# Kernel tuning notes

Hardware: AMD Instinct MI355X
Metric: run time of the kernel (lower is better)

Reference implementation:

```python
import jax, jax.numpy as jnp
import numpy as np


def setup_inputs() -> dict:
    key = jax.random.key(0)
    ks = jax.random.split(key, 8)
    B, C, H, W = 16, 256, 64, 64
    E, heads, R = 256, 8, 64
    s = 0.02  # small init scale in lieu of xavier
    return {
        "x": jax.random.normal(ks[0], (B, C, H, W), dtype=jnp.float32),
        "Wqkv": jax.random.normal(ks[1], (3 * E, C), dtype=jnp.float32) * s,
        "bqkv": jnp.zeros((3 * E,), dtype=jnp.float32),
        "Wr": jax.random.normal(ks[2], (2 * R * heads, C), dtype=jnp.float32) * s,
        "br": jnp.zeros((2 * R * heads,), dtype=jnp.float32),
        "Wout": jax.random.normal(ks[3], (C, E), dtype=jnp.float32) * s,
        "bout": jnp.zeros((C,), dtype=jnp.float32),
        "alpha": jax.random.normal(ks[4], (1,), dtype=jnp.float32),
        "num_heads": heads,
        "num_regions": R,
    }


def reference(x, Wqkv, bqkv, Wr, br, Wout, bout, alpha, num_heads, num_regions):
    B, C, H, W = x.shape
    N = H * W
    E = Wqkv.shape[0] // 3
    d = E // num_heads  # head_dim
    xf = x.reshape(B, C, N)  # [B, C, N]

    # qkv 1x1 conv -> [B, 3E, N] -> [B, h, N, 3d] -> q,k,v [B, h, N, d]
    qkv = jnp.einsum("oc,bcn->bon", Wqkv, xf) + bqkv[:, None]
    qkv = qkv.reshape(B, num_heads, 3 * d, N).transpose(0, 1, 3, 2)
    q, k, v = jnp.split(qkv, 3, axis=-1)

    # region projections: 1x1 conv + softmax over the FULL channel axis (2*R*heads)
    r = jnp.einsum("oc,bcn->bon", Wr, xf) + br[:, None]
    r = jax.nn.softmax(r, axis=1)
    r = r.reshape(B, num_heads, 2 * num_regions, N).transpose(0, 1, 3, 2)
    Rq, Rk = jnp.split(r, 2, axis=-1)  # each [B, h, N, R]

    # pool tokens into regions: [B, h, d, R]
    qr = jnp.einsum("bhnd,bhnr->bhdr", q, Rq)
    kr = jnp.einsum("bhnd,bhnr->bhdr", k, Rk)
    vr = jnp.einsum("bhnd,bhnr->bhdr", v, Rk)

    # region-level attention [B, h, Rq, Rk], scaled by sqrt(head_dim)
    logits = jnp.einsum("bhdq,bhdk->bhqk", qr, kr) / jnp.sqrt(jnp.asarray(d, x.dtype))
    attn = jax.nn.softmax(logits, axis=-1)  # dropout is identity at eval

    # values = v_r @ attn^T -> [B, h, d, Rq]; expand back to tokens via Rq^T
    vals = jnp.einsum("bhdk,bhqk->bhdq", vr, attn)
    vals = jnp.einsum("bhdq,bhnq->bhdn", vals, Rq)  # [B, h, d, N]

    vals = vals.reshape(B, E, N)
    out = jnp.einsum("oe,ben->bon", Wout, vals) + bout[:, None]
    out = out.reshape(B, C, H, W)
    return x + alpha * out
```

## Files before the change

### kernel.cpp

```cpp
#include <hip/hip_runtime.h>
#include <cstdint>

typedef unsigned short ushort_t;
typedef __attribute__((ext_vector_type(4))) unsigned short ushort4_t;
typedef __attribute__((ext_vector_type(8))) unsigned short ushort8_t;
typedef __attribute__((ext_vector_type(8))) __bf16 bf16x8;
typedef __attribute__((ext_vector_type(4))) float f32x4;

constexpr int NB = 16;
constexpr int NC = 256;
constexpr int NN = 4096;
constexpr int NP = 1024;
constexpr int NT = 512;
constexpr int NO = 768;

static __device__ __forceinline__ ushort_t f2b(float f) {
  uint32_t u = __builtin_bit_cast(uint32_t, f);
  u += 0x7FFFu + ((u >> 16) & 1u);
  return (ushort_t)(u >> 16);
}
static __device__ __forceinline__ float b2f(ushort_t h) {
  return __builtin_bit_cast(float, (uint32_t)h << 16);
}
static __device__ __forceinline__ f32x4 mfma16(bf16x8 a, bf16x8 b, f32x4 c) {
  return __builtin_amdgcn_mfma_f32_16x16x32_bf16(a, b, c, 0, 0, 0);
}
typedef __attribute__((address_space(1))) const unsigned int guint;
typedef __attribute__((address_space(3))) unsigned int luint;
static __device__ __forceinline__ void glds16(const void* g, void* l) {
  __builtin_amdgcn_global_load_lds((guint*)g, (luint*)l, 16, 0, 0);
}

template <int KITERS>
__device__ __forceinline__ void gemm_core_sb(const ushort_t* __restrict__ Asrc, size_t lda,
                                             const ushort_t* __restrict__ Bsrc, size_t ldb,
                                             ushort_t* SH, f32x4 (&acc)[4][4], int tid) {
  const int l = tid & 63, w = tid >> 6;
  const int fr = l & 15, kq = (l >> 4) * 8;
  const int rr = l >> 3;
  const int sc = ((l & 7) ^ rr) << 3;
  const int swz = (fr & 7) << 3;
  const int wm = (w >> 1) * 64, wn = (w & 1) * 64;
  ushort_t* As = SH;
  ushort_t* Bs = SH + 8192;
#pragma unroll 1
  for (int it = 0; it < KITERS; it++) {
    const size_t k0 = (size_t)it * 64;
#pragma unroll
    for (int i = 0; i < 4; i++) {
      const int row = i * 32 + w * 8 + rr;
      glds16(Asrc + (size_t)row * lda + k0 + sc, As + (i * 32 + w * 8) * 64);
      glds16(Bsrc + (size_t)row * ldb + k0 + sc, Bs + (i * 32 + w * 8) * 64);
    }
    __syncthreads();
#pragma unroll
    for (int ks = 0; ks < 2; ks++) {
      const int col = ks * 32 + kq;
      bf16x8 af[4], bf[4];
#pragma unroll
      for (int f = 0; f < 4; f++) {
        af[f] = *(const bf16x8*)&As[(wm + f * 16 + fr) * 64 + (col ^ swz)];
        bf[f] = *(const bf16x8*)&Bs[(wn + f * 16 + fr) * 64 + (col ^ swz)];
      }
#pragma unroll
      for (int fm = 0; fm < 4; fm++)
#pragma unroll
        for (int fn = 0; fn < 4; fn++)
          acc[fm][fn] = mfma16(af[fm], bf[fn], acc[fm][fn]);
    }
    __syncthreads();
  }
}

__global__ __launch_bounds__(256) void k0_cvt(const float* __restrict__ x,
                                              ushort_t* __restrict__ xb,
                                              ushort_t* __restrict__ xt) {
  __shared__ ushort_t tr[64][88];
  const int tid = threadIdx.x;
  const int n0 = blockIdx.x * 64, c0 = blockIdx.y * 64, b = blockIdx.z;
  const int cr = (tid >> 4) * 4;
  const int nc4 = (tid & 15) * 4;
#pragma unroll
  for (int i = 0; i < 4; i++) {
    size_t idx = ((size_t)b * NC + c0 + cr + i) * NN + n0 + nc4;
    float4 v = *(const float4*)(x + idx);
    ushort4_t o;
    o[0] = f2b(v.x); o[1] = f2b(v.y); o[2] = f2b(v.z); o[3] = f2b(v.w);
    *(ushort4_t*)(xb + idx) = o;
    tr[nc4 + 0][cr + i] = o[0];
    tr[nc4 + 1][cr + i] = o[1];
    tr[nc4 + 2][cr + i] = o[2];
    tr[nc4 + 3][cr + i] = o[3];
  }
  __syncthreads();
  const int nr = tid >> 2, cc0 = (tid & 3) * 16;
  size_t odx = ((size_t)b * NN + n0 + nr) * NC + c0 + cc0;
  *(ushort8_t*)(xt + odx) = *(const ushort8_t*)&tr[nr][cc0];
  *(ushort8_t*)(xt + odx + 8) = *(const ushort8_t*)&tr[nr][cc0 + 8];
}

__global__ __launch_bounds__(256) void cvt_f2b_k(const float* __restrict__ src,
                                                 ushort_t* __restrict__ dst) {
  int i = (blockIdx.x * 256 + threadIdx.x) * 4;
  float4 v = *(const float4*)(src + i);
  ushort4_t o;
  o[0] = f2b(v.x); o[1] = f2b(v.y); o[2] = f2b(v.z); o[3] = f2b(v.w);
  *(ushort4_t*)(dst + i) = o;
}

__global__ __launch_bounds__(512) void k1_proj(const ushort_t* __restrict__ Wrb,
                                               const ushort_t* __restrict__ xt,
                                               const float* __restrict__ br,
                                               ushort_t* __restrict__ P) {
  __shared__ __align__(16) ushort_t SH[32768];
  const int tid = threadIdx.x;
  const int ord = blockIdx.x;
  const int L = (ord & 7) * 128 + (ord >> 3);
  const int m0 = (L & 3) * 256;
  const int n0 = ((L >> 2) & 15) * 256;
  const int b = L >> 6;
  const int l = tid & 63, w = tid >> 6;
  const int wr = w >> 2, wc = w & 3;
  const int fr = l & 15, kq = (l >> 4) * 8;
  const int swz = (fr & 7) << 3;
  ushort_t* As = SH;
  ushort_t* Bs = SH + 16384;
  const ushort_t* Asrc = Wrb + (size_t)m0 * NC;
  const ushort_t* Bsrc = xt + ((size_t)b * NN + n0) * NC;
  f32x4 acc[8][4] = {};
#pragma unroll 1
  for (int k0 = 0; k0 < NC; k0 += 64) {
#pragma unroll
    for (int rnd = 0; rnd < 4; rnd++) {
      const int rbase = rnd * 64 + w * 8;
      const int row = rbase + (l >> 3);
      const int sc = ((l & 7) ^ (row & 7)) << 3;
      glds16(Asrc + (size_t)row * NC + k0 + sc, As + rbase * 64);
      glds16(Bsrc + (size_t)row * NC + k0 + sc, Bs + rbase * 64);
    }
    __syncthreads();
#pragma unroll
    for (int ks = 0; ks < 2; ks++) {
      const int col = ks * 32 + kq;
      bf16x8 af[8], bf[4];
#pragma unroll
      for (int f = 0; f < 8; f++)
        af[f] = *(const bf16x8*)&As[(wr * 128 + f * 16 + fr) * 64 + (col ^ swz)];
#pragma unroll
      for (int f = 0; f < 4; f++)
        bf[f] = *(const bf16x8*)&Bs[(wc * 64 + f * 16 + fr) * 64 + (col ^ swz)];
#pragma unroll
      for (int fm = 0; fm < 8; fm++)
#pragma unroll
        for (int fn = 0; fn < 4; fn++)
          acc[fm][fn] = mfma16(af[fm], bf[fn], acc[fm][fn]);
    }
    __syncthreads();
  }
  const int colc = l & 15, rb = (l >> 4) * 4;
#pragma unroll
  for (int pp = 0; pp < 4; pp++) {
    if (wr == (pp >> 1)) {
      const int fmb = (pp & 1) * 4;
#pragma unroll
      for (int fm = 0; fm < 4; fm++)
#pragma unroll
        for (int rg = 0; rg < 4; rg++) {
          const int rl = fm * 16 + rb + rg;
          const float bias = br[m0 + pp * 64 + rl];
#pragma unroll
          for (int fn = 0; fn < 4; fn++)
            SH[rl * 264 + wc * 64 + fn * 16 + colc] = f2b(acc[fmb + fm][fn][rg] + bias);
        }
    }
    __syncthreads();
    const int orow = tid >> 3, c8 = (tid & 7) * 32;
    ushort_t* dst = P + ((size_t)b * NP + m0 + pp * 64 + orow) * NN + n0 + c8;
    const ushort_t* s = &SH[orow * 264 + c8];
#pragma unroll
    for (int j = 0; j < 4; j++)
      *(ushort8_t*)(dst + j * 8) = *(const ushort8_t*)(s + j * 8);
    __syncthreads();
  }
}

__global__ __launch_bounds__(512) void k2_softmax(ushort_t* __restrict__ P,
                                                  float* __restrict__ sPpart) {
  __shared__ float red[64][64];
  __shared__ float Mf[64], If[64];
  const int tid = threadIdx.x;
  const int n0 = blockIdx.x * 64, b = blockIdx.y;
  const int cg = tid & 7, pg = tid >> 3;
  ushort_t* base = P + (size_t)b * NP * NN + n0 + cg * 8;

  ushort8_t v[16];
  float m[8];
#pragma unroll
  for (int j = 0; j < 8; j++) m[j] = -3.0e38f;
#pragma unroll
  for (int r = 0; r < 16; r++) {
    v[r] = *(const ushort8_t*)(base + (size_t)(pg * 16 + r) * NN);
#pragma unroll
    for (int j = 0; j < 8; j++) m[j] = fmaxf(m[j], b2f(v[r][j]));
  }
#pragma unroll
  for (int j = 0; j < 8; j++) red[pg][cg * 8 + j] = m[j];
  __syncthreads();
  if (tid < 64) {
    float M = -3.0e38f;
    for (int g = 0; g < 64; g++) M = fmaxf(M, red[g][tid]);
    Mf[tid] = M;
  }
  __syncthreads();
  float mj[8], s[8];
#pragma unroll
  for (int j = 0; j < 8; j++) { mj[j] = Mf[cg * 8 + j]; s[j] = 0.f; }
#pragma unroll
  for (int r = 0; r < 16; r++)
#pragma unroll
    for (int j = 0; j < 8; j++) s[j] += __expf(b2f(v[r][j]) - mj[j]);
#pragma unroll
  for (int j = 0; j < 8; j++) red[pg][cg * 8 + j] = s[j];
  __syncthreads();
  if (tid < 64) {
    float S = 0.f;
    for (int g = 0; g < 64; g++) S += red[g][tid];
    If[tid] = 1.f / S;
  }
  __syncthreads();
  float ij[8];
#pragma unroll
  for (int j = 0; j < 8; j++) ij[j] = If[cg * 8 + j];
#pragma unroll
  for (int r = 0; r < 16; r++) {
    int p = pg * 16 + r;
    ushort8_t o;
    float rs = 0.f;
#pragma unroll
    for (int j = 0; j < 8; j++) {
      float e = __expf(b2f(v[r][j]) - mj[j]) * ij[j];
      o[j] = f2b(e);
      rs += e;
    }
    *(ushort8_t*)(base + (size_t)p * NN) = o;
    rs += __shfl_xor(rs, 1, 64);
    rs += __shfl_xor(rs, 2, 64);
    rs += __shfl_xor(rs, 4, 64);
    if (cg == 0) sPpart[((size_t)blockIdx.x * NB + b) * NP + p] = rs;
  }
}

__global__ __launch_bounds__(256) void k2r_reduce(const float* __restrict__ sPpart,
                                                  float* __restrict__ sP) {
  int idx = blockIdx.x * 256 + threadIdx.x;
  float s = 0.f;
#pragma unroll 8
  for (int bx = 0; bx < 64; bx++) s += sPpart[(size_t)bx * (NB * NP) + idx];
  sP[idx] = s;
}

__global__ __launch_bounds__(256) void k3_pool(const ushort_t* __restrict__ xb,
                                               const ushort_t* __restrict__ P,
                                               ushort_t* __restrict__ XRbT) {
  __shared__ __align__(16) ushort_t SH[4 * 8192];
  const int tid = threadIdx.x;
  const int ord = blockIdx.x;
  const int L = (ord & 7) * 32 + (ord >> 3);
  const int m0 = (L & 1) * 128;
  const int n0 = ((L >> 1) & 7) * 128;
  const int b = L >> 4;
  const int l = tid & 63, w = tid >> 6;
  const int fr = l & 15, kq = (l >> 4) * 8;
  const int rr = l >> 3;
  const int sc = ((l & 7) ^ rr) << 3;
  const int swz = (fr & 7) << 3;
  const int wm = (w >> 1) * 64, wn = (w & 1) * 64;
  const ushort_t* Asrc = xb + ((size_t)b * NC + m0) * NN;
  const ushort_t* Bsrc = P + ((size_t)b * NP + n0) * NN;
  f32x4 acc[4][4] = {};

  auto STAGE = [&](int bi, size_t k0) {
    ushort_t* Ad = SH + bi * 8192;
    ushort_t* Bd = SH + 16384 + bi * 8192;
#pragma unroll
    for (int i = 0; i < 4; i++) {
      const int row = i * 32 + w * 8 + rr;
      glds16(Asrc + (size_t)row * NN + k0 + sc, Ad + (i * 32 + w * 8) * 64);
      glds16(Bsrc + (size_t)row * NN + k0 + sc, Bd + (i * 32 + w * 8) * 64);
    }
  };

  STAGE(0, 0);
  __syncthreads();
  int cur = 0;
#pragma unroll 1
  for (int it = 0; it < 64; it++) {
    if (it + 1 < 64) STAGE(cur ^ 1, (size_t)(it + 1) * 64);
    const ushort_t* Ar = SH + cur * 8192;
    const ushort_t* Br = SH + 16384 + cur * 8192;
#pragma unroll
    for (int ks = 0; ks < 2; ks++) {
      const int col = ks * 32 + kq;
      bf16x8 af[4], bf[4];
#pragma unroll
      for (int f = 0; f < 4; f++) {
        af[f] = *(const bf16x8*)&Ar[(wm + f * 16 + fr) * 64 + (col ^ swz)];
        bf[f] = *(const bf16x8*)&Br[(wn + f * 16 + fr) * 64 + (col ^ swz)];
      }
#pragma unroll
      for (int fm = 0; fm < 4; fm++)
#pragma unroll
        for (int fn = 0; fn < 4; fn++)
          acc[fm][fn] = mfma16(af[fm], bf[fn], acc[fm][fn]);
    }
    __syncthreads();
    cur ^= 1;
  }
  const int colc = l & 15, rb = (l >> 4) * 4;
#pragma unroll
  for (int pp = 0; pp < 2; pp++) {
    if ((w & 1) == pp) {
#pragma unroll
      for (int fm = 0; fm < 4; fm++)
#pragma unroll
        for (int rg = 0; rg < 4; rg++) {
          const int cl = wm + fm * 16 + rb + rg;
#pragma unroll
          for (int fn = 0; fn < 4; fn++) {
            const int pl = fn * 16 + colc;
            SH[pl * 136 + cl] = f2b(acc[fm][fn][rg]);
          }
        }
    }
    __syncthreads();
    const int prow = tid >> 2, cch = (tid & 3) * 32;
    ushort_t* dst = XRbT + ((size_t)b * NP + n0 + pp * 64 + prow) * NC + m0 + cch;
    const ushort_t* s = &SH[prow * 136 + cch];
#pragma unroll
    for (int j = 0; j < 4; j++)
      *(ushort8_t*)(dst + j * 8) = *(const ushort8_t*)(s + j * 8);
    __syncthreads();
  }
}

__global__ __launch_bounds__(256) void k4a_qkvr(const ushort_t* __restrict__ Wqkvb,
                                                const ushort_t* __restrict__ XRbT,
                                                const float* __restrict__ bqkv,
                                                const float* __restrict__ sP,
                                                ushort_t* __restrict__ QKVRb) {
  __shared__ __align__(16) ushort_t SH[2 * 8192];
  const int tid = threadIdx.x;
  const int ord = blockIdx.x;
  const int L = (ord & 7) * 96 + (ord >> 3);
  const int m0 = (L % 6) * 128;
  const int rest = L / 6;
  const int n0 = (rest & 7) * 128;
  const int b = rest >> 3;
  const int lane = tid & 63, w = tid >> 6;
  const int wm = (w >> 1) * 64, wn = (w & 1) * 64;
  f32x4 acc[4][4] = {};
  gemm_core_sb<4>(Wqkvb + (size_t)m0 * NC, NC,
                  XRbT + ((size_t)b * NP + n0) * NC, NC, SH, acc, tid);
  const int col = lane & 15, rb = (lane >> 4) * 4;
  float spv[4];
#pragma unroll
  for (int fn = 0; fn < 4; fn++) spv[fn] = sP[(size_t)b * NP + n0 + wn + fn * 16 + col];
#pragma unroll
  for (int fm = 0; fm < 4; fm++)
#pragma unroll
    for (int rg = 0; rg < 4; rg++) {
      int row = m0 + wm + fm * 16 + rb + rg;
      float bq = bqkv[row];
#pragma unroll
      for (int fn = 0; fn < 4; fn++) {
        int cc = n0 + wn + fn * 16 + col;
        QKVRb[((size_t)b * NO + row) * NP + cc] = f2b(acc[fm][fn][rg] + bq * spv[fn]);
      }
    }
}

__global__ __launch_bounds__(256) void k4b_attn(const ushort_t* __restrict__ QKVRb,
                                                const float* __restrict__ Wout,
                                                ushort_t* __restrict__ Tmb) {
  const int b = blockIdx.x >> 3, h = blockIdx.x & 7;
  const int tid = threadIdx.x;
  __shared__ float qf[96][64];
  __shared__ float attn_sT[64][65];
  __shared__ float vals_s[32][64];
#pragma unroll
  for (int i = 0; i < 3; i++) {
    int u = i * 256 + tid;
    int rw = u >> 3, jc = (u & 7) * 8;
    int p0 = h * 128 + ((rw < 32) ? 0 : 64);
    ushort8_t v = *(const ushort8_t*)(QKVRb + ((size_t)b * NO + h * 96 + rw) * NP + p0 + jc);
#pragma unroll
    for (int j = 0; j < 8; j++) qf[rw][jc + j] = b2f(v[j]);
  }
  __syncthreads();
  const int lj = tid & 63;
  const int rq = tid >> 6;
  float kcol[32];
#pragma unroll
  for (int dd = 0; dd < 32; dd++) kcol[dd] = qf[32 + dd][lj];
  const float isc = 0.17677669529663687f;
#pragma unroll
  for (int r = 0; r < 16; r++) {
    int qi = r * 4 + rq;
    float a = 0.f;
#pragma unroll
    for (int dd = 0; dd < 32; dd++) a += qf[dd][qi] * kcol[dd];
    attn_sT[lj][qi] = a * isc;
  }
  __syncthreads();
  if (tid < 64) {
    float m = -3e38f;
    for (int k = 0; k < 64; k++) m = fmaxf(m, attn_sT[k][tid]);
    float s = 0.f;
    for (int k = 0; k < 64; k++) {
      float e = __expf(attn_sT[k][tid] - m);
      attn_sT[k][tid] = e;
      s += e;
    }
    float inv = 1.f / s;
    for (int k = 0; k < 64; k++) attn_sT[k][tid] *= inv;
  }
  __syncthreads();
  float acol[64];
#pragma unroll
  for (int k = 0; k < 64; k++) acol[k] = attn_sT[k][lj];
#pragma unroll
  for (int r = 0; r < 8; r++) {
    int dd = r * 4 + rq;
    float a = 0.f;
#pragma unroll
    for (int k = 0; k < 64; k++) a += qf[64 + dd][k] * acol[k];
    vals_s[dd][lj] = a;
  }
  __syncthreads();
  float vcol[32];
#pragma unroll
  for (int dd = 0; dd < 32; dd++) vcol[dd] = vals_s[dd][lj];
  for (int r = 0; r < 64; r++) {
    int c = r * 4 + rq;
    const float4* wp = (const float4*)(Wout + (size_t)c * NC + h * 32);
    float a = 0.f;
#pragma unroll
    for (int t = 0; t < 8; t++) {
      float4 w = wp[t];
      a += w.x * vcol[t * 4] + w.y * vcol[t * 4 + 1] + w.z * vcol[t * 4 + 2] +
           w.w * vcol[t * 4 + 3];
    }
    Tmb[((size_t)b * NC + c) * NT + h * 64 + lj] = f2b(a);
  }
}

__global__ __launch_bounds__(256) void k5_out(const float* __restrict__ x,
                                              const ushort_t* __restrict__ P,
                                              const ushort_t* __restrict__ Tmb,
                                              const float* __restrict__ bout,
                                              const float* __restrict__ alpha,
                                              float* __restrict__ out) {
  __shared__ __align__(16) ushort_t Ash[2 * 8192];
  __shared__ __align__(16) ushort_t Bsh[2 * 9216];
  const int tid = threadIdx.x;
  const int ord = blockIdx.x;
  const int L = (ord & 7) * 128 + (ord >> 3);
  const int m0 = (L & 1) * 128;
  const int n0 = ((L >> 1) & 31) * 128;
  const int b = L >> 6;
  const int lane = tid & 63, w = tid >> 6;
  const int wm = (w >> 1) * 64, wn = (w & 1) * 64;
  const int fr = lane & 15, kq = (lane >> 4) * 8;
  const int rr = lane >> 3, sc = ((lane & 7) ^ rr) << 3;
  const int swz = (fr & 7) << 3;
  const ushort_t* Asrc = Tmb + ((size_t)b * NC + m0) * NT;
  const int kg = tid >> 5, ng = (tid & 31) * 4;
  f32x4 acc[4][4] = {};
  ushort4_t bv[8];

  auto A_STAGE = [&](int bi, int k0) {
    ushort_t* Ad = Ash + bi * 8192;
#pragma unroll
    for (int i = 0; i < 4; i++) {
      const int row = i * 32 + w * 8 + rr;
      glds16(Asrc + (size_t)row * NT + k0 + sc, Ad + (i * 32 + w * 8) * 64);
    }
  };
  auto B_LOAD = [&](int k0) {
#pragma unroll
    for (int i = 0; i < 8; i++) {
      int hj = k0 + kg * 8 + i;
      int prow = ((hj >> 6) << 7) + (hj & 63);
      bv[i] = *(const ushort4_t*)(P + ((size_t)b * NP + prow) * NN + n0 + ng);
    }
  };
  auto B_WRITE = [&](int bi) {
#pragma unroll
    for (int jj = 0; jj < 4; jj++) {
      ushort8_t pk;
#pragma unroll
      for (int i = 0; i < 8; i++) pk[i] = bv[i][jj];
      *(ushort8_t*)&Bsh[bi * 9216 + (ng + jj) * 72 + kg * 8] = pk;
    }
  };

  A_STAGE(0, 0);
  B_LOAD(0);
  B_WRITE(0);
  __syncthreads();
  int cur = 0;
#pragma unroll 1
  for (int it = 0; it < 8; it++) {
    if (it + 1 < 8) {
      A_STAGE(cur ^ 1, (it + 1) * 64);
      B_LOAD((it + 1) * 64);
    }
    const ushort_t* Ar = Ash + cur * 8192;
    const ushort_t* Br = Bsh + cur * 9216;
#pragma unroll
    for (int ks = 0; ks < 2; ks++) {
      const int col = ks * 32 + kq;
      bf16x8 af[4], bf[4];
#pragma unroll
      for (int f = 0; f < 4; f++) {
        af[f] = *(const bf16x8*)&Ar[(wm + f * 16 + fr) * 64 + (col ^ swz)];
        bf[f] = *(const bf16x8*)&Br[(wn + f * 16 + fr) * 72 + col];
      }
#pragma unroll
      for (int fm = 0; fm < 4; fm++)
#pragma unroll
        for (int fn = 0; fn < 4; fn++)
          acc[fm][fn] = mfma16(af[fm], bf[fn], acc[fm][fn]);
    }
    if (it + 1 < 8) B_WRITE(cur ^ 1);
    __syncthreads();
    cur ^= 1;
  }
  const float al = alpha[0];
  const int col = lane & 15, rb = (lane >> 4) * 4;
#pragma unroll
  for (int fm = 0; fm < 4; fm++)
#pragma unroll
    for (int rg = 0; rg < 4; rg++) {
      int row = m0 + wm + fm * 16 + rb + rg;
      float bias = bout[row];
#pragma unroll
      for (int fn = 0; fn < 4; fn++) {
        int cc = n0 + wn + fn * 16 + col;
        size_t idx = ((size_t)b * NC + row) * NN + cc;
        out[idx] = x[idx] + al * (acc[fm][fn][rg] + bias);
      }
    }
}

extern "C" void kernel_launch(void* const* d_in, const int* in_sizes, int n_in,
                              void* d_out, int out_size, void* d_ws, size_t ws_size,
                              hipStream_t stream) {
  const float* x = (const float*)d_in[0];
  const float* Wqkv = (const float*)d_in[1];
  const float* bqkv = (const float*)d_in[2];
  const float* Wr = (const float*)d_in[3];
  const float* br = (const float*)d_in[4];
  const float* Wout = (const float*)d_in[5];
  const float* bout = (const float*)d_in[6];
  const float* alpha = (const float*)d_in[7];
  float* out = (float*)d_out;

  char* ws = (char*)d_ws;
  ushort_t* P = (ushort_t*)ws;
  ushort_t* xb = (ushort_t*)(ws + 134217728);
  ushort_t* QKVRb = (ushort_t*)(ws + 134217728);
  ushort_t* xt = (ushort_t*)(ws + 167772160);
  ushort_t* XRbT = (ushort_t*)(ws + 167772160);
  ushort_t* Wrb = (ushort_t*)(ws + 201326592);
  float* sPpart = (float*)(ws + 201850880);
  ushort_t* Wqkvb = (ushort_t*)(ws + 201850880);
  float* sP = (float*)(ws + 206045184);
  ushort_t* Tmb = (ushort_t*)(ws + 206110720);

  k0_cvt<<<dim3(64, 4, 16), 256, 0, stream>>>(x, xb, xt);
  cvt_f2b_k<<<256, 256, 0, stream>>>(Wr, Wrb);
  k1_proj<<<1024, 512, 0, stream>>>(Wrb, xt, br, P);
  k2_softmax<<<dim3(64, 16), 512, 0, stream>>>(P, sPpart);
  k2r_reduce<<<64, 256, 0, stream>>>(sPpart, sP);
  cvt_f2b_k<<<192, 256, 0, stream>>>(Wqkv, Wqkvb);
  k3_pool<<<256, 256, 0, stream>>>(xb, P, XRbT);
  k4a_qkvr<<<768, 256, 0, stream>>>(Wqkvb, XRbT, bqkv, sP, QKVRb);
  k4b_attn<<<128, 256, 0, stream>>>(QKVRb, Wout, Tmb);
  k5_out<<<1024, 256, 0, stream>>>(x, P, Tmb, bout, alpha, out);
}
```

Baseline: 345.0 us.

## Fuse region projection GEMM with channel softmax to keep logits on-chip

Merges the region-projection GEMM and the channel-axis softmax into one kernel, with each block owning 64 tokens across all 1024 output channels. Logits stay packed as bf16 in registers while a running max and sum are reduced through shared memory, so only the normalized probabilities are written to P. This removes one full write and read of the 128MB logits tensor and one launch. In exchange, each block streams the whole Wr matrix in small 128-row chunks with many barriers, and the register footprint may limit occupancy.

```diff
diff --git a/kernel.cpp b/kernel.cpp
--- a/kernel.cpp
+++ b/kernel.cpp
@@ -108,145 +108,157 @@
   *(ushort4_t*)(dst + i) = o;
 }
 
-__global__ __launch_bounds__(512) void k1_proj(const ushort_t* __restrict__ Wrb,
-                                               const ushort_t* __restrict__ xt,
-                                               const float* __restrict__ br,
-                                               ushort_t* __restrict__ P) {
-  __shared__ __align__(16) ushort_t SH[32768];
+__global__ __launch_bounds__(512) void k12_proj_sm(const ushort_t* __restrict__ Wrb,
+                                                   const ushort_t* __restrict__ xt,
+                                                   const float* __restrict__ br,
+                                                   ushort_t* __restrict__ P,
+                                                   float* __restrict__ sPpart) {
+  __shared__ __align__(16) ushort_t xts[64 * 256];
+  __shared__ __align__(16) ushort_t As[128 * 66];
+  __shared__ float red[8][64];
+  __shared__ float Mrun[64], Sinv[64];
   const int tid = threadIdx.x;
-  const int ord = blockIdx.x;
-  const int L = (ord & 7) * 128 + (ord >> 3);
-  const int m0 = (L & 3) * 256;
-  const int n0 = ((L >> 2) & 15) * 256;
-  const int b = L >> 6;
+  const int nblk = blockIdx.x, b = blockIdx.y;
+  const int n0 = nblk * 64;
   const int l = tid & 63, w = tid >> 6;
-  const int wr = w >> 2, wc = w & 3;
-  const int fr = l & 15, kq = (l >> 4) * 8;
-  const int swz = (fr & 7) << 3;
-  ushort_t* As = SH;
-  ushort_t* Bs = SH + 16384;
-  const ushort_t* Asrc = Wrb + (size_t)m0 * NC;
-  const ushort_t* Bsrc = xt + ((size_t)b * NN + n0) * NC;
-  f32x4 acc[8][4] = {};
-#pragma unroll 1
-  for (int k0 = 0; k0 < NC; k0 += 64) {
-#pragma unroll
-    for (int rnd = 0; rnd < 4; rnd++) {
-      const int rbase = rnd * 64 + w * 8;
-      const int row = rbase + (l >> 3);
-      const int sc = ((l & 7) ^ (row & 7)) << 3;
-      glds16(Asrc + (size_t)row * NC + k0 + sc, As + rbase * 64);
-      glds16(Bsrc + (size_t)row * NC + k0 + sc, Bs + rbase * 64);
-    }
-    __syncthreads();
-#pragma unroll
-    for (int ks = 0; ks < 2; ks++) {
-      const int col = ks * 32 + kq;
-      bf16x8 af[8], bf[4];
-#pragma unroll
-      for (int f = 0; f < 8; f++)
-        af[f] = *(const bf16x8*)&As[(wr * 128 + f * 16 + fr) * 64 + (col ^ swz)];
-#pragma unroll
-      for (int f = 0; f < 4; f++)
-        bf[f] = *(const bf16x8*)&Bs[(wc * 64 + f * 16 + fr) * 64 + (col ^ swz)];
-#pragma unroll
-      for (int fm = 0; fm < 8; fm++)
-#pragma unroll
-        for (int fn = 0; fn < 4; fn++)
-          acc[fm][fn] = mfma16(af[fm], bf[fn], acc[fm][fn]);
-    }
-    __syncthreads();
-  }
-  const int colc = l & 15, rb = (l >> 4) * 4;
-#pragma unroll
-  for (int pp = 0; pp < 4; pp++) {
-    if (wr == (pp >> 1)) {
-      const int fmb = (pp & 1) * 4;
-#pragma unroll
-      for (int fm = 0; fm < 4; fm++)
-#pragma unroll
-        for (int rg = 0; rg < 4; rg++) {
-          const int rl = fm * 16 + rb + rg;
-          const float bias = br[m0 + pp * 64 + rl];
-#pragma unroll
-          for (int fn = 0; fn < 4; fn++)
-            SH[rl * 264 + wc * 64 + fn * 16 + colc] = f2b(acc[fmb + fm][fn][rg] + bias);
+  const int col = l & 15, lg = l >> 4;
+  const int kq = lg * 8;
+  const int swz = (col & 7) << 3;
+
+#pragma unroll
+  for (int j = 0; j < 4; j++) {
+    int unit = tid + j * 512;
+    int n = unit >> 5, k8 = (unit & 31) * 8;
+    ushort8_t v = *(const ushort8_t*)(xt + ((size_t)b * NN + n0 + n) * NC + k8);
+    *(ushort8_t*)&xts[n * 256 + (k8 ^ ((n & 7) << 3))] = v;
+  }
+
+  uint32_t st[8][4][2];
+#pragma unroll
+  for (int pc = 0; pc < 8; pc++) {
+    f32x4 acc[4] = {};
+#pragma unroll
+    for (int it = 0; it < 4; it++) {
+#pragma unroll
+      for (int i = 0; i < 2; i++) {
+        const int rbase = i * 64 + w * 8;
+        const int row = rbase + (l >> 3);
+        const int sc = ((l & 7) ^ (row & 7)) << 3;
+        glds16(Wrb + (size_t)(pc * 128 + row) * NC + it * 64 + sc, As + rbase * 64);
+      }
+      __syncthreads();
+#pragma unroll
+      for (int ks = 0; ks < 2; ks++) {
+        const int cc = ks * 32 + kq;
+        bf16x8 af = *(const bf16x8*)&As[(w * 16 + col) * 64 + (cc ^ swz)];
+#pragma unroll
+        for (int fn = 0; fn < 4; fn++) {
+          bf16x8 bf = *(const bf16x8*)&xts[(fn * 16 + col) * 256 + it * 64 + (cc ^ swz)];
+          acc[fn] = mfma16(af, bf, acc[fn]);
         }
-    }
-    __syncthreads();
-    const int orow = tid >> 3, c8 = (tid & 7) * 32;
-    ushort_t* dst = P + ((size_t)b * NP + m0 + pp * 64 + orow) * NN + n0 + c8;
-    const ushort_t* s = &SH[orow * 264 + c8];
-#pragma unroll
-    for (int j = 0; j < 4; j++)
-      *(ushort8_t*)(dst + j * 8) = *(const ushort8_t*)(s + j * 8);
-    __syncthreads();
-  }
-}
-
-__global__ __launch_bounds__(512) void k2_softmax(ushort_t* __restrict__ P,
-                                                  float* __restrict__ sPpart) {
-  __shared__ float red[64][64];
-  __shared__ float Mf[64], If[64];
-  const int tid = threadIdx.x;
-  const int n0 = blockIdx.x * 64, b = blockIdx.y;
-  const int cg = tid & 7, pg = tid >> 3;
-  ushort_t* base = P + (size_t)b * NP * NN + n0 + cg * 8;
-
-  ushort8_t v[16];
-  float m[8];
-#pragma unroll
-  for (int j = 0; j < 8; j++) m[j] = -3.0e38f;
-#pragma unroll
-  for (int r = 0; r < 16; r++) {
-    v[r] = *(const ushort8_t*)(base + (size_t)(pg * 16 + r) * NN);
-#pragma unroll
-    for (int j = 0; j < 8; j++) m[j] = fmaxf(m[j], b2f(v[r][j]));
-  }
-#pragma unroll
-  for (int j = 0; j < 8; j++) red[pg][cg * 8 + j] = m[j];
-  __syncthreads();
-  if (tid < 64) {
-    float M = -3.0e38f;
-    for (int g = 0; g < 64; g++) M = fmaxf(M, red[g][tid]);
-    Mf[tid] = M;
-  }
-  __syncthreads();
-  float mj[8], s[8];
-#pragma unroll
-  for (int j = 0; j < 8; j++) { mj[j] = Mf[cg * 8 + j]; s[j] = 0.f; }
-#pragma unroll
-  for (int r = 0; r < 16; r++)
-#pragma unroll
-    for (int j = 0; j < 8; j++) s[j] += __expf(b2f(v[r][j]) - mj[j]);
-#pragma unroll
-  for (int j = 0; j < 8; j++) red[pg][cg * 8 + j] = s[j];
+      }
+      __syncthreads();
+    }
+    const float4 brv = *(const float4*)(br + pc * 128 + w * 16 + lg * 4);
+    float mx[4];
+#pragma unroll
+    for (int fn = 0; fn < 4; fn++) {
+      float v0 = acc[fn][0] + brv.x;
+      float v1 = acc[fn][1] + brv.y;
+      float v2 = acc[fn][2] + brv.z;
+      float v3 = acc[fn][3] + brv.w;
+      st[pc][fn][0] = ((uint32_t)f2b(v1) << 16) | f2b(v0);
+      st[pc][fn][1] = ((uint32_t)f2b(v3) << 16) | f2b(v2);
+      mx[fn] = fmaxf(fmaxf(v0, v1), fmaxf(v2, v3));
+    }
+#pragma unroll
+    for (int fn = 0; fn < 4; fn++) {
+      mx[fn] = fmaxf(mx[fn], __shfl_xor(mx[fn], 16, 64));
+      mx[fn] = fmaxf(mx[fn], __shfl_xor(mx[fn], 32, 64));
+    }
+    if (lg == 0) {
+#pragma unroll
+      for (int fn = 0; fn < 4; fn++) red[w][fn * 16 + col] = mx[fn];
+    }
+    __syncthreads();
+    if (tid < 64) {
+      float m8 = red[0][tid];
+#pragma unroll
+      for (int g = 1; g < 8; g++) m8 = fmaxf(m8, red[g][tid]);
+      Mrun[tid] = (pc == 0) ? m8 : fmaxf(Mrun[tid], m8);
+    }
+  }
+  __syncthreads();
+  float Mn[4], ssum[4];
+#pragma unroll
+  for (int fn = 0; fn < 4; fn++) { Mn[fn] = Mrun[fn * 16 + col]; ssum[fn] = 0.f; }
+#pragma unroll
+  for (int pc = 0; pc < 8; pc++)
+#pragma unroll
+    for (int fn = 0; fn < 4; fn++)
+#pragma unroll
+      for (int j = 0; j < 2; j++) {
+        uint32_t u = st[pc][fn][j];
+        float e0 = __expf(b2f((ushort_t)(u & 0xFFFFu)) - Mn[fn]);
+        float e1 = __expf(b2f((ushort_t)(u >> 16)) - Mn[fn]);
+        st[pc][fn][j] = ((uint32_t)f2b(e1) << 16) | f2b(e0);
+        ssum[fn] += e0 + e1;
+      }
+#pragma unroll
+  for (int fn = 0; fn < 4; fn++) {
+    ssum[fn] += __shfl_xor(ssum[fn], 16, 64);
+    ssum[fn] += __shfl_xor(ssum[fn], 32, 64);
+  }
+  if (lg == 0) {
+#pragma unroll
+    for (int fn = 0; fn < 4; fn++) red[w][fn * 16 + col] = ssum[fn];
+  }
   __syncthreads();
   if (tid < 64) {
     float S = 0.f;
-    for (int g = 0; g < 64; g++) S += red[g][tid];
-    If[tid] = 1.f / S;
-  }
-  __syncthreads();
-  float ij[8];
-#pragma unroll
-  for (int j = 0; j < 8; j++) ij[j] = If[cg * 8 + j];
-#pragma unroll
-  for (int r = 0; r < 16; r++) {
-    int p = pg * 16 + r;
-    ushort8_t o;
-    float rs = 0.f;
-#pragma unroll
-    for (int j = 0; j < 8; j++) {
-      float e = __expf(b2f(v[r][j]) - mj[j]) * ij[j];
-      o[j] = f2b(e);
-      rs += e;
-    }
-    *(ushort8_t*)(base + (size_t)p * NN) = o;
-    rs += __shfl_xor(rs, 1, 64);
-    rs += __shfl_xor(rs, 2, 64);
-    rs += __shfl_xor(rs, 4, 64);
-    if (cg == 0) sPpart[((size_t)blockIdx.x * NB + b) * NP + p] = rs;
+#pragma unroll
+    for (int g = 0; g < 8; g++) S += red[g][tid];
+    Sinv[tid] = 1.f / S;
+  }
+  __syncthreads();
+  float sv[4];
+#pragma unroll
+  for (int fn = 0; fn < 4; fn++) sv[fn] = Sinv[fn * 16 + col];
+#pragma unroll
+  for (int pc = 0; pc < 8; pc++) {
+    float rsum[4] = {0.f, 0.f, 0.f, 0.f};
+#pragma unroll
+    for (int fn = 0; fn < 4; fn++)
+#pragma unroll
+      for (int j = 0; j < 2; j++) {
+        uint32_t u = st[pc][fn][j];
+        float p0 = b2f((ushort_t)(u & 0xFFFFu)) * sv[fn];
+        float p1 = b2f((ushort_t)(u >> 16)) * sv[fn];
+        const int rl = w * 16 + lg * 4 + j * 2;
+        As[rl * 66 + fn * 16 + col] = f2b(p0);
+        As[(rl + 1) * 66 + fn * 16 + col] = f2b(p1);
+        rsum[j * 2] += p0;
+        rsum[j * 2 + 1] += p1;
+      }
+#pragma unroll
+    for (int rg = 0; rg < 4; rg++) {
+      rsum[rg] += __shfl_xor(rsum[rg], 1, 64);
+      rsum[rg] += __shfl_xor(rsum[rg], 2, 64);
+      rsum[rg] += __shfl_xor(rsum[rg], 4, 64);
+      rsum[rg] += __shfl_xor(rsum[rg], 8, 64);
+    }
+    if (col == 0) {
+      const int pbase = pc * 128 + w * 16 + lg * 4;
+      *(float4*)&sPpart[((size_t)nblk * NB + b) * NP + pbase] =
+          make_float4(rsum[0], rsum[1], rsum[2], rsum[3]);
+    }
+    __syncthreads();
+    const int row = tid >> 2, q = tid & 3;
+    const ushort_t* s = &As[row * 66 + q * 16];
+    ushort_t* dst = P + ((size_t)b * NP + pc * 128 + row) * NN + n0 + q * 16;
+    *(ushort8_t*)(dst) = *(const ushort8_t*)(s);
+    *(ushort8_t*)(dst + 8) = *(const ushort8_t*)(s + 8);
+    __syncthreads();
   }
 }
 
@@ -580,8 +592,7 @@
 
   k0_cvt<<<dim3(64, 4, 16), 256, 0, stream>>>(x, xb, xt);
   cvt_f2b_k<<<256, 256, 0, stream>>>(Wr, Wrb);
-  k1_proj<<<1024, 512, 0, stream>>>(Wrb, xt, br, P);
-  k2_softmax<<<dim3(64, 16), 512, 0, stream>>>(P, sPpart);
+  k12_proj_sm<<<dim3(64, 16), 512, 0, stream>>>(Wrb, xt, br, P, sPpart);
   k2r_reduce<<<64, 256, 0, stream>>>(sPpart, sP);
   cvt_f2b_k<<<192, 256, 0, stream>>>(Wqkv, Wqkvb);
   k3_pool<<<256, 256, 0, stream>>>(xb, P, XRbT);
```

Measured after the change: 383.1 us. 1.11x slower.

## Retile region projection GEMM to 128x128 blocks using shared gemm core

Applied to the files above, without the earlier changes.

The region projection kernel moves from 256x256 tiles with 512 threads to 128x128 tiles with 256 threads, launching four times as many blocks. It reuses an existing shared GEMM helper (gemm_core_sb) in place of the hand-written inline loop. The epilogue now stages one 128-row tile through shared memory and writes it out in a single pass. This aims to raise occupancy and cut LDS use per block, at the cost of less operand reuse per tile and more global traffic for the weight and activation tiles.

```diff
diff --git a/kernel.cpp b/kernel.cpp
--- a/kernel.cpp
+++ b/kernel.cpp
@@ -108,80 +108,40 @@
   *(ushort4_t*)(dst + i) = o;
 }
 
-__global__ __launch_bounds__(512) void k1_proj(const ushort_t* __restrict__ Wrb,
+__global__ __launch_bounds__(256) void k1_proj(const ushort_t* __restrict__ Wrb,
                                                const ushort_t* __restrict__ xt,
                                                const float* __restrict__ br,
                                                ushort_t* __restrict__ P) {
-  __shared__ __align__(16) ushort_t SH[32768];
+  __shared__ __align__(16) ushort_t SH[17408];
   const int tid = threadIdx.x;
   const int ord = blockIdx.x;
-  const int L = (ord & 7) * 128 + (ord >> 3);
-  const int m0 = (L & 3) * 256;
-  const int n0 = ((L >> 2) & 15) * 256;
-  const int b = L >> 6;
-  const int l = tid & 63, w = tid >> 6;
-  const int wr = w >> 2, wc = w & 3;
-  const int fr = l & 15, kq = (l >> 4) * 8;
-  const int swz = (fr & 7) << 3;
-  ushort_t* As = SH;
-  ushort_t* Bs = SH + 16384;
-  const ushort_t* Asrc = Wrb + (size_t)m0 * NC;
-  const ushort_t* Bsrc = xt + ((size_t)b * NN + n0) * NC;
-  f32x4 acc[8][4] = {};
-#pragma unroll 1
-  for (int k0 = 0; k0 < NC; k0 += 64) {
-#pragma unroll
-    for (int rnd = 0; rnd < 4; rnd++) {
-      const int rbase = rnd * 64 + w * 8;
-      const int row = rbase + (l >> 3);
-      const int sc = ((l & 7) ^ (row & 7)) << 3;
-      glds16(Asrc + (size_t)row * NC + k0 + sc, As + rbase * 64);
-      glds16(Bsrc + (size_t)row * NC + k0 + sc, Bs + rbase * 64);
-    }
-    __syncthreads();
-#pragma unroll
-    for (int ks = 0; ks < 2; ks++) {
-      const int col = ks * 32 + kq;
-      bf16x8 af[8], bf[4];
-#pragma unroll
-      for (int f = 0; f < 8; f++)
-        af[f] = *(const bf16x8*)&As[(wr * 128 + f * 16 + fr) * 64 + (col ^ swz)];
-#pragma unroll
-      for (int f = 0; f < 4; f++)
-        bf[f] = *(const bf16x8*)&Bs[(wc * 64 + f * 16 + fr) * 64 + (col ^ swz)];
-#pragma unroll
-      for (int fm = 0; fm < 8; fm++)
-#pragma unroll
-        for (int fn = 0; fn < 4; fn++)
-          acc[fm][fn] = mfma16(af[fm], bf[fn], acc[fm][fn]);
-    }
-    __syncthreads();
-  }
-  const int colc = l & 15, rb = (l >> 4) * 4;
-#pragma unroll
-  for (int pp = 0; pp < 4; pp++) {
-    if (wr == (pp >> 1)) {
-      const int fmb = (pp & 1) * 4;
-#pragma unroll
-      for (int fm = 0; fm < 4; fm++)
-#pragma unroll
-        for (int rg = 0; rg < 4; rg++) {
-          const int rl = fm * 16 + rb + rg;
-          const float bias = br[m0 + pp * 64 + rl];
-#pragma unroll
-          for (int fn = 0; fn < 4; fn++)
-            SH[rl * 264 + wc * 64 + fn * 16 + colc] = f2b(acc[fmb + fm][fn][rg] + bias);
-        }
-    }
-    __syncthreads();
-    const int orow = tid >> 3, c8 = (tid & 7) * 32;
-    ushort_t* dst = P + ((size_t)b * NP + m0 + pp * 64 + orow) * NN + n0 + c8;
-    const ushort_t* s = &SH[orow * 264 + c8];
-#pragma unroll
-    for (int j = 0; j < 4; j++)
-      *(ushort8_t*)(dst + j * 8) = *(const ushort8_t*)(s + j * 8);
-    __syncthreads();
-  }
+  const int L = (ord & 7) * 512 + (ord >> 3);
+  const int m0 = (L & 7) * 128;
+  const int n0 = ((L >> 3) & 31) * 128;
+  const int b = L >> 8;
+  const int lane = tid & 63, w = tid >> 6;
+  const int wm = (w >> 1) * 64, wn = (w & 1) * 64;
+  f32x4 acc[4][4] = {};
+  gemm_core_sb<4>(Wrb + (size_t)m0 * NC, NC,
+                  xt + ((size_t)b * NN + n0) * NC, NC, SH, acc, tid);
+  const int colc = lane & 15, rb = (lane >> 4) * 4;
+#pragma unroll
+  for (int fm = 0; fm < 4; fm++)
+#pragma unroll
+    for (int rg = 0; rg < 4; rg++) {
+      const int row = wm + fm * 16 + rb + rg;
+      const float bias = br[m0 + row];
+#pragma unroll
+      for (int fn = 0; fn < 4; fn++)
+        SH[row * 136 + wn + fn * 16 + colc] = f2b(acc[fm][fn][rg] + bias);
+    }
+  __syncthreads();
+  const int orow = tid >> 1, half = tid & 1;
+  const ushort_t* s = &SH[orow * 136 + half * 64];
+  ushort_t* dst = P + ((size_t)b * NP + m0 + orow) * NN + n0 + half * 64;
+#pragma unroll
+  for (int j = 0; j < 8; j++)
+    *(ushort8_t*)(dst + j * 8) = *(const ushort8_t*)(s + j * 8);
 }
 
 __global__ __launch_bounds__(512) void k2_softmax(ushort_t* __restrict__ P,
@@ -580,7 +540,7 @@
 
   k0_cvt<<<dim3(64, 4, 16), 256, 0, stream>>>(x, xb, xt);
   cvt_f2b_k<<<256, 256, 0, stream>>>(Wr, Wrb);
-  k1_proj<<<1024, 512, 0, stream>>>(Wrb, xt, br, P);
+  k1_proj<<<4096, 256, 0, stream>>>(Wrb, xt, br, P);
   k2_softmax<<<dim3(64, 16), 512, 0, stream>>>(P, sPpart);
   k2r_reduce<<<64, 256, 0, stream>>>(sPpart, sP);
   cvt_f2b_k<<<192, 256, 0, stream>>>(Wqkv, Wqkvb);
```

After: 339.4 us. No clear change (-1.6%).
